# Optimization experiments

Measured on AMD Instinct MI355X. Metric: run time of the kernel, lower is better.

The kernel has to match this reference:

```python
import jax, jax.numpy as jnp
import numpy as np

D_MODEL = 1024
N_HEADS = 16
D_FF = 4096
EPS = 1e-5


def _linear_init(key, fan_in, fan_out):
    # torch nn.Linear default: U(-1/sqrt(fan_in), 1/sqrt(fan_in))
    k1, k2 = jax.random.split(key)
    bound = 1.0 / np.sqrt(fan_in)
    W = jax.random.uniform(k1, (fan_in, fan_out), minval=-bound, maxval=bound, dtype=jnp.float32)
    b = jax.random.uniform(k2, (fan_out,), minval=-bound, maxval=bound, dtype=jnp.float32)
    return W, b


def setup_inputs() -> dict:
    key = jax.random.key(0)
    ks = jax.random.split(key, 8)
    x = jax.random.normal(ks[0], (4, 2048, D_MODEL), dtype=jnp.float32)
    Wq, bq = _linear_init(ks[1], D_MODEL, D_MODEL)
    Wk, bk = _linear_init(ks[2], D_MODEL, D_MODEL)
    Wv, bv = _linear_init(ks[3], D_MODEL, D_MODEL)
    Wo, bo = _linear_init(ks[4], D_MODEL, D_MODEL)
    W1, b1 = _linear_init(ks[5], D_MODEL, D_FF)
    W2, b2 = _linear_init(ks[6], D_FF, D_MODEL)
    g1 = jnp.ones((D_MODEL,), jnp.float32); be1 = jnp.zeros((D_MODEL,), jnp.float32)
    g2 = jnp.ones((D_MODEL,), jnp.float32); be2 = jnp.zeros((D_MODEL,), jnp.float32)
    return {"x": x, "Wq": Wq, "bq": bq, "Wk": Wk, "bk": bk, "Wv": Wv, "bv": bv,
            "Wo": Wo, "bo": bo, "g1": g1, "be1": be1, "W1": W1, "b1": b1,
            "W2": W2, "b2": b2, "g2": g2, "be2": be2}


def _layernorm(x, g, b):
    mu = jnp.mean(x, axis=-1, keepdims=True)
    var = jnp.mean(jnp.square(x - mu), axis=-1, keepdims=True)
    return (x - mu) * jax.lax.rsqrt(var + EPS) * g + b


def reference(x, Wq, bq, Wk, bk, Wv, bv, Wo, bo, g1, be1, W1, b1, W2, b2, g2, be2):
    B, T, D = x.shape
    H, dk = N_HEADS, D // N_HEADS
    # projections -> [B, H, T, dk]
    def split_heads(y):
        return y.reshape(B, T, H, dk).transpose(0, 2, 1, 3)
    Q = split_heads(x @ Wq + bq)
    K = split_heads(x @ Wk + bk)
    V = split_heads(x @ Wv + bv)
    scores = jnp.einsum('bhtd,bhsd->bhts', Q, K) / jnp.sqrt(jnp.float32(dk))
    weights = jax.nn.softmax(scores, axis=-1)  # no causal mask in original
    ctx = jnp.einsum('bhts,bhsd->bhtd', weights, V)
    ctx = ctx.transpose(0, 2, 1, 3).reshape(B, T, D)
    attn_out = ctx @ Wo + bo
    x = _layernorm(x + attn_out, g1, be1)
    ff = jax.nn.relu(x @ W1 + b1) @ W2 + b2
    x = _layernorm(x + ff, g2, be2)
    return x
```

## Files before the change

kernel.cpp:

```cpp
#include <hip/hip_runtime.h>
#include <hip/hip_bf16.h>
#include <stdint.h>

typedef __attribute__((ext_vector_type(8))) short short8;
typedef __attribute__((ext_vector_type(4))) float f32x4;
typedef __attribute__((ext_vector_type(16))) float f32x16;

#define SEQ 2048
#define DMODEL 1024
#define NH 16
#define DKH 64

__device__ __forceinline__ uint16_t f2b(float f) {
  uint32_t u = __float_as_uint(f);
  uint32_t r = (u + 0x7fff + ((u >> 16) & 1)) >> 16;
  return (uint16_t)r;
}

__device__ __forceinline__ void gload16(const uint16_t* g, uint16_t* l) {
  __builtin_amdgcn_global_load_lds((const __attribute__((address_space(1))) void*)g,
                                   (__attribute__((address_space(3))) void*)l, 16, 0, 0);
}

__global__ __launch_bounds__(256) void k_castx(const float* __restrict__ x,
                                               uint16_t* __restrict__ xb) {
  int i = blockIdx.x * 256 + threadIdx.x;
  float4 v = reinterpret_cast<const float4*>(x)[i];
  uint16_t o[4] = {f2b(v.x), f2b(v.y), f2b(v.z), f2b(v.w)};
  reinterpret_cast<uint2*>(xb)[i] = *reinterpret_cast<uint2*>(o);
}

__global__ __launch_bounds__(256) void k_tcast(const float* __restrict__ W,
                                               uint16_t* __restrict__ Wt, int K, int N) {
  __shared__ float tile[32][33];
  int n0 = blockIdx.x * 32, k0 = blockIdx.y * 32;
  int tx = threadIdx.x & 31, ty = threadIdx.x >> 5;
#pragma unroll
  for (int i = 0; i < 32; i += 8)
    tile[ty + i][tx] = W[(size_t)(k0 + ty + i) * N + n0 + tx];
  __syncthreads();
#pragma unroll
  for (int i = 0; i < 32; i += 8)
    Wt[(size_t)(n0 + ty + i) * K + k0 + tx] = f2b(tile[tx][ty + i]);
}

__global__ __launch_bounds__(256) void k_vtrans(const uint16_t* __restrict__ V,
                                                uint16_t* __restrict__ Vt) {
  __shared__ uint16_t tile[64][72];
  const int s0 = blockIdx.x * 64;
  const uint16_t* Vp = V + (size_t)blockIdx.y * SEQ * DKH;
  uint16_t* Vtp = Vt + (size_t)blockIdx.y * SEQ * DKH;
  const int t = threadIdx.x;
#pragma unroll
  for (int i = t; i < 512; i += 256) {
    int r = i >> 3, c8 = (i & 7) << 3;
    *reinterpret_cast<uint4*>(&tile[r][c8]) =
        *reinterpret_cast<const uint4*>(Vp + (size_t)(s0 + r) * DKH + c8);
  }
  __syncthreads();
#pragma unroll
  for (int i = t; i < 512; i += 256) {
    int d = i >> 3, s8 = (i & 7) << 3;
    uint16_t tmp[8];
#pragma unroll
    for (int j = 0; j < 8; ++j) tmp[j] = tile[s8 + j][d];
    *reinterpret_cast<uint4*>(Vtp + (size_t)d * SEQ + s0 + s8) = *reinterpret_cast<uint4*>(tmp);
  }
}

#define MODE_QKV 0
#define MODE_RES 1
#define MODE_RELU 2

template <int MODE>
__global__ __launch_bounds__(256) void k_gemm(
    const uint16_t* __restrict__ A, const uint16_t* __restrict__ Bt, int M, int N, int K,
    const float* __restrict__ bias0, const float* __restrict__ bias1,
    const float* __restrict__ bias2, const float* __restrict__ res,
    uint16_t* __restrict__ ob0, uint16_t* __restrict__ ob1, uint16_t* __restrict__ ob2,
    float* __restrict__ of) {
  __shared__ __align__(16) uint16_t As[128 * 32];
  __shared__ __align__(16) uint16_t Bs[128 * 32];
  const int brow = blockIdx.y << 7, bcol = blockIdx.x << 7;
  const int t = threadIdx.x;
  const int wave = t >> 6, lane = t & 63;
  const int g = lane >> 4, lr = lane & 15;
  const int wr = (wave >> 1) << 6, wc = (wave & 1) << 6;

  const int i0 = t, i1 = t + 256;
  const uint16_t* gA0 = A + (size_t)(brow + (i0 >> 2)) * K + ((i0 & 3) << 3);
  const uint16_t* gA1 = A + (size_t)(brow + (i1 >> 2)) * K + ((i1 & 3) << 3);
  const uint16_t* gB0 = Bt + (size_t)(bcol + (i0 >> 2)) * K + ((i0 & 3) << 3);
  const uint16_t* gB1 = Bt + (size_t)(bcol + (i1 >> 2)) * K + ((i1 & 3) << 3);
  uint16_t* lA0 = As + i0 * 8;
  uint16_t* lA1 = As + i1 * 8;
  uint16_t* lB0 = Bs + i0 * 8;
  uint16_t* lB1 = Bs + i1 * 8;

  f32x4 acc[4][4] = {};

  for (int k0 = 0; k0 < K; k0 += 32) {
    __syncthreads();
    gload16(gA0 + k0, lA0);
    gload16(gA1 + k0, lA1);
    gload16(gB0 + k0, lB0);
    gload16(gB1 + k0, lB1);
    __syncthreads();
    short8 af[4], bf[4];
#pragma unroll
    for (int m = 0; m < 4; ++m)
      af[m] = *reinterpret_cast<const short8*>(&As[(wr + m * 16 + lr) * 32 + g * 8]);
#pragma unroll
    for (int n = 0; n < 4; ++n)
      bf[n] = *reinterpret_cast<const short8*>(&Bs[(wc + n * 16 + lr) * 32 + g * 8]);
#pragma unroll
    for (int m = 0; m < 4; ++m)
#pragma unroll
      for (int n = 0; n < 4; ++n)
        acc[m][n] = __builtin_amdgcn_mfma_f32_16x16x32_bf16(af[m], bf[n], acc[m][n], 0, 0, 0);
  }

#pragma unroll
  for (int m = 0; m < 4; ++m) {
#pragma unroll
    for (int n = 0; n < 4; ++n) {
#pragma unroll
      for (int q = 0; q < 4; ++q) {
        int r = brow + wr + m * 16 + g * 4 + q;
        int c = bcol + wc + n * 16 + lr;
        float v = acc[m][n][q];
        if (MODE == MODE_QKV) {
          int which = c >> 10;
          int hd = c & 1023;
          const float* bp = which == 0 ? bias0 : (which == 1 ? bias1 : bias2);
          v += bp[hd];
          if (which == 0) v *= 0.1803368801f;
          uint16_t* dst = which == 0 ? ob0 : (which == 1 ? ob1 : ob2);
          int b = r >> 11, tt = r & 2047;
          int h = hd >> 6, d = hd & 63;
          dst[((size_t)((b * NH + h) * SEQ + tt)) * DKH + d] = f2b(v);
        } else if (MODE == MODE_RES) {
          size_t idx = (size_t)r * N + c;
          of[idx] = v + bias0[c] + res[idx];
        } else {
          v += bias0[c];
          v = fmaxf(v, 0.0f);
          ob0[(size_t)r * N + c] = f2b(v);
        }
      }
    }
  }
}

__global__ __launch_bounds__(256) void k_attn(const uint16_t* __restrict__ Qb,
                                              const uint16_t* __restrict__ Kb,
                                              const uint16_t* __restrict__ Vtg,
                                              uint16_t* __restrict__ ctx) {
  __shared__ __align__(16) uint16_t Ks[2][64 * 64];
  __shared__ __align__(16) uint16_t Vs[2][64 * 64];
  __shared__ float l_arr[4][32];
  const int bh = blockIdx.x;
  const int b = bh >> 4, h = bh & 15;
  const uint16_t* Qp = Qb + (size_t)bh * SEQ * DKH;
  const uint16_t* Kp = Kb + (size_t)bh * SEQ * DKH;
  const uint16_t* Vp = Vtg + (size_t)bh * SEQ * DKH;
  const int t = threadIdx.x, w = t >> 6, l = t & 63;
  const int lo5 = l & 31, hh = l >> 5;
  const int qbase = blockIdx.y * 128 + w * 32;

  short8 qf[4];
#pragma unroll
  for (int kc = 0; kc < 4; ++kc)
    qf[kc] = *reinterpret_cast<const short8*>(Qp + (size_t)(qbase + lo5) * DKH + kc * 16 + hh * 8);

  f32x16 oacc[2] = {};
  float lsum = 0.f;

  const int swz = ((l & 7) ^ ((l >> 3) & 7)) << 3;
  const int ci0 = w * 2, ci1 = w * 2 + 1;
  const int r0 = ci0 * 8 + (l >> 3), r1 = ci1 * 8 + (l >> 3);
  uint16_t* ldsK0 = &Ks[0][0] + ci0 * 512 + l * 8;
  uint16_t* ldsK1 = &Ks[0][0] + ci1 * 512 + l * 8;
  uint16_t* ldsV0 = &Vs[0][0] + ci0 * 512 + l * 8;
  uint16_t* ldsV1 = &Vs[0][0] + ci1 * 512 + l * 8;
  const uint16_t* gK0 = Kp + (size_t)r0 * DKH + swz;
  const uint16_t* gK1 = Kp + (size_t)r1 * DKH + swz;
  const uint16_t* gV0 = Vp + (size_t)r0 * SEQ + swz;
  const uint16_t* gV1 = Vp + (size_t)r1 * SEQ + swz;

  gload16(gK0, ldsK0);
  gload16(gK1, ldsK1);
  gload16(gV0, ldsV0);
  gload16(gV1, ldsV1);
  __syncthreads();

  for (int tile = 0; tile < 32; ++tile) {
    const int cur = tile & 1;
    if (tile < 31) {
      const int nxt = (cur ^ 1) * 4096;
      const size_t s0n = (size_t)(tile + 1) * 64;
      gload16(gK0 + s0n * DKH, ldsK0 + nxt);
      gload16(gK1 + s0n * DKH, ldsK1 + nxt);
      gload16(gV0 + s0n, ldsV0 + nxt);
      gload16(gV1 + s0n, ldsV1 + nxt);
    }
    const char* Kbuf = reinterpret_cast<const char*>(&Ks[cur][0]);
    const char* Vbuf = reinterpret_cast<const char*>(&Vs[cur][0]);

#pragma unroll
    for (int sblk = 0; sblk < 2; ++sblk) {
      short8 kf[4];
      const int krow = sblk * 32 + lo5;
      const int kxor = (krow & 7) << 4;
#pragma unroll
      for (int kc = 0; kc < 4; ++kc) {
        int cb = (kc * 32 + hh * 16) ^ kxor;
        kf[kc] = *reinterpret_cast<const short8*>(Kbuf + krow * 128 + cb);
      }
      short8 vf[2][2];
#pragma unroll
      for (int scl = 0; scl < 2; ++scl)
#pragma unroll
        for (int dblk = 0; dblk < 2; ++dblk) {
          int vrow = dblk * 32 + lo5;
          int cb = (sblk * 64 + scl * 32 + hh * 16) ^ ((vrow & 7) << 4);
          vf[scl][dblk] = *reinterpret_cast<const short8*>(Vbuf + vrow * 128 + cb);
        }

      f32x16 sa = {};
      __builtin_amdgcn_s_setprio(1);
#pragma unroll
      for (int kc = 0; kc < 4; ++kc)
        sa = __builtin_amdgcn_mfma_f32_32x32x16_bf16(kf[kc], qf[kc], sa, 0, 0, 0);
      __builtin_amdgcn_s_setprio(0);

      float p[16];
      float ls = 0.f;
#pragma unroll
      for (int r = 0; r < 16; ++r) {
        p[r] = __builtin_amdgcn_exp2f(sa[r]);
        ls += p[r];
      }
      lsum += ls;

      uint32_t clo[4], chi[4];
#pragma unroll
      for (int m = 0; m < 4; ++m) {
        asm("v_cvt_pk_bf16_f32 %0, %1, %2" : "=v"(clo[m]) : "v"(p[4 * m]), "v"(p[4 * m + 1]));
        asm("v_cvt_pk_bf16_f32 %0, %1, %2" : "=v"(chi[m]) : "v"(p[4 * m + 2]), "v"(p[4 * m + 3]));
      }

#pragma unroll
      for (int scl = 0; scl < 2; ++scl) {
        uint32_t a0 = clo[2 * scl], b0 = clo[2 * scl + 1];
        uint32_t a1 = chi[2 * scl], b1 = chi[2 * scl + 1];
        asm("v_permlane32_swap_b32 %0, %1" : "+v"(a0), "+v"(b0));
        asm("v_permlane32_swap_b32 %0, %1" : "+v"(a1), "+v"(b1));
        union {
          uint32_t u[4];
          short8 s;
        } pu;
        pu.u[0] = a0;
        pu.u[1] = a1;
        pu.u[2] = b0;
        pu.u[3] = b1;
        __builtin_amdgcn_s_setprio(1);
#pragma unroll
        for (int dblk = 0; dblk < 2; ++dblk)
          oacc[dblk] = __builtin_amdgcn_mfma_f32_32x32x16_bf16(pu.s, vf[scl][dblk], oacc[dblk], 0, 0, 0);
        __builtin_amdgcn_s_setprio(0);
      }
    }
    __syncthreads();
  }

  {
    float full = lsum + __shfl_xor(lsum, 32, 64);
    if (l < 32) l_arr[w][lo5] = full;
  }
#pragma unroll
  for (int r = 0; r < 16; ++r) {
    int q = (r & 3) + 8 * (r >> 2) + 4 * hh;
    float li = 1.0f / l_arr[w][q];
    int rowg = b * SEQ + qbase + q;
#pragma unroll
    for (int dblk = 0; dblk < 2; ++dblk) {
      int colg = h * DKH + dblk * 32 + lo5;
      ctx[(size_t)rowg * DMODEL + colg] = f2b(oacc[dblk][r] * li);
    }
  }
}

template <bool WRITE_B>
__global__ __launch_bounds__(256) void k_ln(const float* __restrict__ in,
                                            const float* __restrict__ gam,
                                            const float* __restrict__ bet,
                                            float* __restrict__ outf,
                                            uint16_t* __restrict__ outb) {
  const int row = blockIdx.x;
  const int t = threadIdx.x, lane = t & 63, w = t >> 6;
  const float* p = in + (size_t)row * DMODEL;
  float4 v = reinterpret_cast<const float4*>(p)[t];
  float s = v.x + v.y + v.z + v.w;
  float s2 = v.x * v.x + v.y * v.y + v.z * v.z + v.w * v.w;
#pragma unroll
  for (int off = 1; off < 64; off <<= 1) {
    s += __shfl_xor(s, off, 64);
    s2 += __shfl_xor(s2, off, 64);
  }
  __shared__ float rs[4], rq[4];
  if (lane == 0) {
    rs[w] = s;
    rq[w] = s2;
  }
  __syncthreads();
  float ts = rs[0] + rs[1] + rs[2] + rs[3];
  float tq = rq[0] + rq[1] + rq[2] + rq[3];
  const float inv = 1.0f / DMODEL;
  float mu = ts * inv;
  float var = tq * inv - mu * mu;
  float rstd = rsqrtf(var + 1e-5f);
  float4 gg = reinterpret_cast<const float4*>(gam)[t];
  float4 bb = reinterpret_cast<const float4*>(bet)[t];
  float4 y;
  y.x = (v.x - mu) * rstd * gg.x + bb.x;
  y.y = (v.y - mu) * rstd * gg.y + bb.y;
  y.z = (v.z - mu) * rstd * gg.z + bb.z;
  y.w = (v.w - mu) * rstd * gg.w + bb.w;
  reinterpret_cast<float4*>(outf)[(size_t)row * 256 + t] = y;
  if (WRITE_B) {
    uint16_t o[4] = {f2b(y.x), f2b(y.y), f2b(y.z), f2b(y.w)};
    reinterpret_cast<uint2*>(outb)[(size_t)row * 256 + t] = *reinterpret_cast<uint2*>(o);
  }
}

extern "C" void kernel_launch(void* const* d_in, const int* in_sizes, int n_in, void* d_out,
                              int out_size, void* d_ws, size_t ws_size, hipStream_t stream) {
  const float* x = (const float*)d_in[0];
  const float* Wq = (const float*)d_in[1];
  const float* bq = (const float*)d_in[2];
  const float* Wk = (const float*)d_in[3];
  const float* bk = (const float*)d_in[4];
  const float* Wv = (const float*)d_in[5];
  const float* bv = (const float*)d_in[6];
  const float* Wo = (const float*)d_in[7];
  const float* bo = (const float*)d_in[8];
  const float* g1 = (const float*)d_in[9];
  const float* be1 = (const float*)d_in[10];
  const float* W1 = (const float*)d_in[11];
  const float* b1 = (const float*)d_in[12];
  const float* W2 = (const float*)d_in[13];
  const float* b2 = (const float*)d_in[14];
  const float* g2 = (const float*)d_in[15];
  const float* be2 = (const float*)d_in[16];

  char* ws = (char*)d_ws;
  size_t off = 0;
  auto alloc = [&](size_t bytes) {
    char* p = ws + off;
    off += (bytes + 255) & ~(size_t)255;
    return p;
  };
  uint16_t* wt_qkv = (uint16_t*)alloc(3072ull * 1024 * 2);
  uint16_t* wt_o = (uint16_t*)alloc(1024ull * 1024 * 2);
  uint16_t* wt_1 = (uint16_t*)alloc(4096ull * 1024 * 2);
  uint16_t* wt_2 = (uint16_t*)alloc(1024ull * 4096 * 2);
  uint16_t* xb = (uint16_t*)alloc(8192ull * 1024 * 2);
  float* sum1 = (float*)alloc(8192ull * 1024 * 4);
  float* x1f = (float*)alloc(8192ull * 1024 * 4);
  char* big = alloc(16777216ull + 67108864ull);
  uint16_t* Qbuf = (uint16_t*)big;
  uint16_t* Kbuf = (uint16_t*)(big + 16777216ull);
  uint16_t* Vbuf = (uint16_t*)(big + 2 * 16777216ull);
  uint16_t* vt = (uint16_t*)x1f;
  uint16_t* ctx = xb;
  uint16_t* x1b = (uint16_t*)big;
  uint16_t* hbuf = (uint16_t*)(big + 16777216ull);
  (void)ws_size;

  k_tcast<<<dim3(32, 32), 256, 0, stream>>>(Wq, wt_qkv, 1024, 1024);
  k_tcast<<<dim3(32, 32), 256, 0, stream>>>(Wk, wt_qkv + 1024 * 1024, 1024, 1024);
  k_tcast<<<dim3(32, 32), 256, 0, stream>>>(Wv, wt_qkv + 2 * 1024 * 1024, 1024, 1024);
  k_tcast<<<dim3(32, 32), 256, 0, stream>>>(Wo, wt_o, 1024, 1024);
  k_tcast<<<dim3(128, 32), 256, 0, stream>>>(W1, wt_1, 1024, 4096);
  k_tcast<<<dim3(32, 128), 256, 0, stream>>>(W2, wt_2, 4096, 1024);
  k_castx<<<8192, 256, 0, stream>>>(x, xb);
  k_gemm<MODE_QKV><<<dim3(24, 64), 256, 0, stream>>>(xb, wt_qkv, 8192, 3072, 1024, bq, bk, bv,
                                                     nullptr, Qbuf, Kbuf, Vbuf, nullptr);
  k_vtrans<<<dim3(32, 64), 256, 0, stream>>>(Vbuf, vt);
  k_attn<<<dim3(64, 16), 256, 0, stream>>>(Qbuf, Kbuf, vt, ctx);
  k_gemm<MODE_RES><<<dim3(8, 64), 256, 0, stream>>>(ctx, wt_o, 8192, 1024, 1024, bo, nullptr,
                                                    nullptr, x, nullptr, nullptr, nullptr, sum1);
  k_ln<true><<<8192, 256, 0, stream>>>(sum1, g1, be1, x1f, x1b);
  k_gemm<MODE_RELU><<<dim3(32, 64), 256, 0, stream>>>(x1b, wt_1, 8192, 4096, 1024, b1, nullptr,
                                                      nullptr, nullptr, hbuf, nullptr, nullptr,
                                                      nullptr);
  k_gemm<MODE_RES><<<dim3(8, 64), 256, 0, stream>>>(hbuf, wt_2, 8192, 1024, 4096, b2, nullptr,
                                                    nullptr, x1f, nullptr, nullptr, nullptr, sum1);
  k_ln<false><<<8192, 256, 0, stream>>>(sum1, g2, be2, (float*)d_out, nullptr);
}
```

Before: 477.6 us.

## Replace GEMM with double-buffered 256-row tiled kernel and move bias/residual into layernorm

Replaces the 128x128, K=32 single-buffered GEMM with a 512-thread kernel that uses 256xBN tiles and K=64 steps. It double-buffers the LDS tiles with XOR-swizzled layout, prefetches the next tile in phases between MFMA groups, and raises MFMA wave priority. The bias and residual addition for the output and FF2 projections moves from the GEMM epilogue into the layernorm kernel, so the GEMM writes raw fp32 results. The larger tiles are meant to raise data reuse and hide global-load latency. The cost is more LDS and register pressure, and fewer blocks for the N=1024 GEMMs.

New measurement: 432.5 us. 9.4% less time.

```diff
diff --git a/kernel.cpp b/kernel.cpp
--- a/kernel.cpp
+++ b/kernel.cpp
@@ -69,66 +69,115 @@
 }
 
 #define MODE_QKV 0
-#define MODE_RES 1
+#define MODE_RAW 1
 #define MODE_RELU 2
 
-template <int MODE>
-__global__ __launch_bounds__(256) void k_gemm(
+template <int BN, int MODE>
+__global__ __launch_bounds__(512, 2) void k_gemm2(
     const uint16_t* __restrict__ A, const uint16_t* __restrict__ Bt, int M, int N, int K,
     const float* __restrict__ bias0, const float* __restrict__ bias1,
-    const float* __restrict__ bias2, const float* __restrict__ res,
-    uint16_t* __restrict__ ob0, uint16_t* __restrict__ ob1, uint16_t* __restrict__ ob2,
-    float* __restrict__ of) {
-  __shared__ __align__(16) uint16_t As[128 * 32];
-  __shared__ __align__(16) uint16_t Bs[128 * 32];
-  const int brow = blockIdx.y << 7, bcol = blockIdx.x << 7;
+    const float* __restrict__ bias2, uint16_t* __restrict__ ob0, uint16_t* __restrict__ ob1,
+    uint16_t* __restrict__ ob2, float* __restrict__ of) {
+  constexpr int ASZ = 256 * 64;
+  constexpr int BSZ = BN * 64;
+  __shared__ __align__(16) uint16_t lds[2 * (ASZ + BSZ)];
+  uint16_t* const Abase = lds;
+  uint16_t* const Bbase = lds + 2 * ASZ;
+  constexpr int WN = (BN == 256) ? 4 : 2;
+  constexpr int MREP = (BN == 256) ? 8 : 4;
+  constexpr int NPH = (BN == 256) ? 4 : 2;
+  const int brow = blockIdx.y << 8;
+  const int bcol = blockIdx.x * BN;
   const int t = threadIdx.x;
-  const int wave = t >> 6, lane = t & 63;
-  const int g = lane >> 4, lr = lane & 15;
-  const int wr = (wave >> 1) << 6, wc = (wave & 1) << 6;
-
-  const int i0 = t, i1 = t + 256;
-  const uint16_t* gA0 = A + (size_t)(brow + (i0 >> 2)) * K + ((i0 & 3) << 3);
-  const uint16_t* gA1 = A + (size_t)(brow + (i1 >> 2)) * K + ((i1 & 3) << 3);
-  const uint16_t* gB0 = Bt + (size_t)(bcol + (i0 >> 2)) * K + ((i0 & 3) << 3);
-  const uint16_t* gB1 = Bt + (size_t)(bcol + (i1 >> 2)) * K + ((i1 & 3) << 3);
-  uint16_t* lA0 = As + i0 * 8;
-  uint16_t* lA1 = As + i1 * 8;
-  uint16_t* lB0 = Bs + i0 * 8;
-  uint16_t* lB1 = Bs + i1 * 8;
-
-  f32x4 acc[4][4] = {};
-
-  for (int k0 = 0; k0 < K; k0 += 32) {
-    __syncthreads();
-    gload16(gA0 + k0, lA0);
-    gload16(gA1 + k0, lA1);
-    gload16(gB0 + k0, lB0);
-    gload16(gB1 + k0, lB1);
-    __syncthreads();
-    short8 af[4], bf[4];
-#pragma unroll
-    for (int m = 0; m < 4; ++m)
-      af[m] = *reinterpret_cast<const short8*>(&As[(wr + m * 16 + lr) * 32 + g * 8]);
-#pragma unroll
-    for (int n = 0; n < 4; ++n)
-      bf[n] = *reinterpret_cast<const short8*>(&Bs[(wc + n * 16 + lr) * 32 + g * 8]);
-#pragma unroll
-    for (int m = 0; m < 4; ++m)
-#pragma unroll
-      for (int n = 0; n < 4; ++n)
-        acc[m][n] = __builtin_amdgcn_mfma_f32_16x16x32_bf16(af[m], bf[n], acc[m][n], 0, 0, 0);
-  }
-
-#pragma unroll
-  for (int m = 0; m < 4; ++m) {
+  const int wid = t >> 6, l = t & 63, g = l >> 4, lr = l & 15;
+  const int wr = wid / WN, wc = wid % WN;
+  const int wrow = wr * (MREP * 16);
+  const int wcol = wc * 64;
+
+  const int srow = t >> 3;
+  const int ss0 = (t & 7) ^ (srow & 7);
+  const int ss1 = (t & 7) ^ ((srow + 64) & 7);
+
+  auto stage_half = [&](const uint16_t* gsrc, int grow0, int kk, uint16_t* ldst) {
+    gload16(gsrc + (size_t)(grow0 + srow) * K + kk + ss0 * 8, ldst + t * 8);
+    gload16(gsrc + (size_t)(grow0 + srow + 64) * K + kk + ss1 * 8, ldst + 4096 + t * 8);
+  };
+  auto rdfrag = [&](const uint16_t* buf, int ar, int kk) -> short8 {
+    int slot = ((kk << 2) + g) ^ (ar & 7);
+    return *reinterpret_cast<const short8*>(buf + ar * 64 + slot * 8);
+  };
+
+  f32x4 acc[MREP][4] = {};
+  const int nt = K >> 6;
+
+  stage_half(A, brow, 0, Abase);
+  stage_half(A, brow + 128, 0, Abase + 8192);
+  stage_half(Bt, bcol, 0, Bbase);
+  if (BN == 256) stage_half(Bt, bcol + 128, 0, Bbase + 8192);
+  __syncthreads();
+
+  for (int kt = 0; kt < nt; ++kt) {
+    const int cur = kt & 1;
+    const uint16_t* Ac = Abase + cur * ASZ;
+    const uint16_t* Bc = Bbase + cur * BSZ;
+    uint16_t* An = Abase + (cur ^ 1) * ASZ;
+    uint16_t* Bn = Bbase + (cur ^ 1) * BSZ;
+    const bool pf = (kt + 1 < nt);
+    const int knx = (kt + 1) << 6;
+#pragma unroll
+    for (int q = 0; q < NPH; ++q) {
+      const int mq = (BN == 256) ? (q >> 1) : 0;
+      const int nq = (BN == 256) ? (q & 1) : q;
+      short8 af[4][2], bf[2][2];
+#pragma unroll
+      for (int j = 0; j < 4; ++j)
+#pragma unroll
+        for (int kk = 0; kk < 2; ++kk)
+          af[j][kk] = rdfrag(Ac, wrow + (mq * 4 + j) * 16 + lr, kk);
+#pragma unroll
+      for (int j = 0; j < 2; ++j)
+#pragma unroll
+        for (int kk = 0; kk < 2; ++kk)
+          bf[j][kk] = rdfrag(Bc, wcol + (nq * 2 + j) * 16 + lr, kk);
+      if (pf) {
+        if (q == 0) {
+          stage_half(A, brow, knx, An);
+          stage_half(A, brow + 128, knx, An + 8192);
+          if (BN == 128) stage_half(Bt, bcol, knx, Bn);
+        }
+        if (BN == 256 && q == 1) stage_half(Bt, bcol, knx, Bn);
+        if (BN == 256 && q == 2) stage_half(Bt, bcol + 128, knx, Bn + 8192);
+      }
+      __builtin_amdgcn_s_barrier();
+      __builtin_amdgcn_s_setprio(1);
+#pragma unroll
+      for (int j = 0; j < 4; ++j)
+#pragma unroll
+        for (int j2 = 0; j2 < 2; ++j2)
+#pragma unroll
+          for (int kk = 0; kk < 2; ++kk)
+            acc[mq * 4 + j][nq * 2 + j2] = __builtin_amdgcn_mfma_f32_16x16x32_bf16(
+                af[j][kk], bf[j2][kk], acc[mq * 4 + j][nq * 2 + j2], 0, 0, 0);
+      __builtin_amdgcn_s_setprio(0);
+      if (q == NPH - 1) {
+        asm volatile("s_waitcnt vmcnt(0)" ::: "memory");
+        __builtin_amdgcn_s_barrier();
+        __builtin_amdgcn_sched_barrier(0);
+      } else {
+        __builtin_amdgcn_s_barrier();
+      }
+    }
+  }
+
+#pragma unroll
+  for (int m = 0; m < MREP; ++m) {
 #pragma unroll
     for (int n = 0; n < 4; ++n) {
 #pragma unroll
-      for (int q = 0; q < 4; ++q) {
-        int r = brow + wr + m * 16 + g * 4 + q;
-        int c = bcol + wc + n * 16 + lr;
-        float v = acc[m][n][q];
+      for (int qi = 0; qi < 4; ++qi) {
+        int r = brow + wrow + m * 16 + g * 4 + qi;
+        int c = bcol + wcol + n * 16 + lr;
+        float v = acc[m][n][qi];
         if (MODE == MODE_QKV) {
           int which = c >> 10;
           int hd = c & 1023;
@@ -139,13 +188,12 @@
           int b = r >> 11, tt = r & 2047;
           int h = hd >> 6, d = hd & 63;
           dst[((size_t)((b * NH + h) * SEQ + tt)) * DKH + d] = f2b(v);
-        } else if (MODE == MODE_RES) {
-          size_t idx = (size_t)r * N + c;
-          of[idx] = v + bias0[c] + res[idx];
-        } else {
+        } else if (MODE == MODE_RELU) {
           v += bias0[c];
           v = fmaxf(v, 0.0f);
           ob0[(size_t)r * N + c] = f2b(v);
+        } else {
+          of[(size_t)r * N + c] = v;
         }
       }
     }
@@ -293,14 +341,21 @@
 
 template <bool WRITE_B>
 __global__ __launch_bounds__(256) void k_ln(const float* __restrict__ in,
+                                            const float* __restrict__ bias,
+                                            const float* __restrict__ res,
                                             const float* __restrict__ gam,
                                             const float* __restrict__ bet,
                                             float* __restrict__ outf,
                                             uint16_t* __restrict__ outb) {
   const int row = blockIdx.x;
   const int t = threadIdx.x, lane = t & 63, w = t >> 6;
-  const float* p = in + (size_t)row * DMODEL;
-  float4 v = reinterpret_cast<const float4*>(p)[t];
+  float4 v = reinterpret_cast<const float4*>(in + (size_t)row * DMODEL)[t];
+  float4 bb0 = reinterpret_cast<const float4*>(bias)[t];
+  float4 rr = reinterpret_cast<const float4*>(res + (size_t)row * DMODEL)[t];
+  v.x += bb0.x + rr.x;
+  v.y += bb0.y + rr.y;
+  v.z += bb0.z + rr.z;
+  v.w += bb0.w + rr.w;
   float s = v.x + v.y + v.z + v.w;
   float s2 = v.x * v.x + v.y * v.y + v.z * v.z + v.w * v.w;
 #pragma unroll
@@ -385,17 +440,16 @@
   k_tcast<<<dim3(128, 32), 256, 0, stream>>>(W1, wt_1, 1024, 4096);
   k_tcast<<<dim3(32, 128), 256, 0, stream>>>(W2, wt_2, 4096, 1024);
   k_castx<<<8192, 256, 0, stream>>>(x, xb);
-  k_gemm<MODE_QKV><<<dim3(24, 64), 256, 0, stream>>>(xb, wt_qkv, 8192, 3072, 1024, bq, bk, bv,
-                                                     nullptr, Qbuf, Kbuf, Vbuf, nullptr);
+  k_gemm2<256, MODE_QKV><<<dim3(12, 32), 512, 0, stream>>>(
+      xb, wt_qkv, 8192, 3072, 1024, bq, bk, bv, Qbuf, Kbuf, Vbuf, nullptr);
   k_vtrans<<<dim3(32, 64), 256, 0, stream>>>(Vbuf, vt);
   k_attn<<<dim3(64, 16), 256, 0, stream>>>(Qbuf, Kbuf, vt, ctx);
-  k_gemm<MODE_RES><<<dim3(8, 64), 256, 0, stream>>>(ctx, wt_o, 8192, 1024, 1024, bo, nullptr,
-                                                    nullptr, x, nullptr, nullptr, nullptr, sum1);
-  k_ln<true><<<8192, 256, 0, stream>>>(sum1, g1, be1, x1f, x1b);
-  k_gemm<MODE_RELU><<<dim3(32, 64), 256, 0, stream>>>(x1b, wt_1, 8192, 4096, 1024, b1, nullptr,
-                                                      nullptr, nullptr, hbuf, nullptr, nullptr,
-                                                      nullptr);
-  k_gemm<MODE_RES><<<dim3(8, 64), 256, 0, stream>>>(hbuf, wt_2, 8192, 1024, 4096, b2, nullptr,
-                                                    nullptr, x1f, nullptr, nullptr, nullptr, sum1);
-  k_ln<false><<<8192, 256, 0, stream>>>(sum1, g2, be2, (float*)d_out, nullptr);
-}
+  k_gemm2<128, MODE_RAW><<<dim3(8, 32), 512, 0, stream>>>(
+      ctx, wt_o, 8192, 1024, 1024, nullptr, nullptr, nullptr, nullptr, nullptr, nullptr, sum1);
+  k_ln<true><<<8192, 256, 0, stream>>>(sum1, bo, x, g1, be1, x1f, x1b);
+  k_gemm2<256, MODE_RELU><<<dim3(16, 32), 512, 0, stream>>>(
+      x1b, wt_1, 8192, 4096, 1024, b1, nullptr, nullptr, hbuf, nullptr, nullptr, nullptr);
+  k_gemm2<128, MODE_RAW><<<dim3(8, 32), 512, 0, stream>>>(
+      hbuf, wt_2, 8192, 1024, 4096, nullptr, nullptr, nullptr, nullptr, nullptr, nullptr, sum1);
+  k_ln<false><<<8192, 256, 0, stream>>>(sum1, b2, x1f, g2, be2, (float*)d_out, nullptr);
+}
```
